# Optimization experiments

Hardware: AMD Instinct MI355X
Metric: run time of the kernel (lower is better)

The kernel has to match this reference:

```python
import jax, jax.numpy as jnp
import numpy as np

B, T, H = 4096, 512, 512
GATE = 2 + H  # concat([x(1), h(H), mask(1)])


def setup_inputs() -> dict:
    key = jax.random.key(0)
    ks = jax.random.split(key, 20)
    s = 1.0 / np.sqrt(GATE)
    inp = {
        "x": jax.random.normal(ks[0], (B, T), jnp.float32),
        "x_last": jax.random.normal(ks[1], (B, T), jnp.float32),
        "interval": jax.random.uniform(ks[2], (B, T), jnp.float32),
        "mask": (jax.random.uniform(ks[3], (B, T)) > 0.3).astype(jnp.float32),
        # gamma decay layers
        "Wgx": jax.random.normal(ks[4], (1, 1), jnp.float32),
        "bgx": jnp.zeros((1,), jnp.float32),
        "Wgh": jax.random.normal(ks[5], (H, 1), jnp.float32),
        "bgh": jnp.zeros((H,), jnp.float32),
        # gate layers: Linear(GATE, H)
        "Wz": jax.random.normal(ks[6], (H, GATE), jnp.float32) * s,
        "bz": jnp.zeros((H,), jnp.float32),
        "Wr": jax.random.normal(ks[7], (H, GATE), jnp.float32) * s,
        "br": jnp.zeros((H,), jnp.float32),
        "Wh": jax.random.normal(ks[8], (H, GATE), jnp.float32) * s,
        "bh": jnp.zeros((H,), jnp.float32),
        # output head Linear(H, 1)
        "Wo": jax.random.normal(ks[9], (1, H), jnp.float32) / np.sqrt(H),
        "bo": jnp.zeros((1,), jnp.float32),
    }
    return inp


def reference(x, x_last, interval, mask, Wgx, bgx, Wgh, bgh,
              Wz, bz, Wr, br, Wh, bh, Wo, bo):
    # x, x_last, interval, mask: [B, T]; feature dim is 1 after unsqueeze
    x3 = x[..., None]            # [B, T, 1]
    xl3 = x_last[..., None]
    it3 = interval[..., None]
    m3 = mask[..., None]
    # mean(x*m, dim=1) * T / sum(m, dim=1) == sum(x*m)/sum(m)
    x_mean = jnp.sum(x3 * m3, axis=1) / jnp.sum(m3, axis=1)  # [B, 1]

    h0 = jnp.zeros((x.shape[0], Wz.shape[0]), x.dtype)
    # time-major stacks for scan: [T, B, 1]
    xs = (jnp.swapaxes(x3, 0, 1), jnp.swapaxes(xl3, 0, 1),
          jnp.swapaxes(m3, 0, 1), jnp.swapaxes(it3, 0, 1))

    def step(h, ts):
        xt, xl, mt, it = ts  # each [B, 1]
        gamma_x = jnp.exp(-jax.nn.relu(it @ Wgx.T + bgx))   # [B, 1]
        gamma_h = jnp.exp(-jax.nn.relu(it @ Wgh.T + bgh))   # [B, H]
        xi = mt * xt + (1.0 - mt) * (gamma_x * xl + (1.0 - gamma_x) * x_mean)
        h = gamma_h * h
        comb = jnp.concatenate([xi, h, mt], axis=1)          # [B, GATE]
        z = jax.nn.sigmoid(comb @ Wz.T + bz)
        r = jax.nn.sigmoid(comb @ Wr.T + br)
        comb_r = jnp.concatenate([xi, r * h, mt], axis=1)
        h_tilde = jnp.tanh(comb_r @ Wh.T + bh)
        h = (1.0 - z) * h + z * h_tilde
        return h, None

    h, _ = jax.lax.scan(step, h0, xs)
    return jax.nn.sigmoid(h @ Wo.T + bo)  # [B, 1]
```

## Files before the change

### kernel.cpp

```cpp
#include <hip/hip_runtime.h>
#include <stdint.h>

#define T_LEN 512
#define H_DIM 512
#define B_TOT 4096
#define GATE_D 514
#define CLUSTERS 16
#define RANKS 16
#define CROWS 256
#define OWNC 32
#define NTHR 512
#define BARPAD 64

typedef short s16x8 __attribute__((ext_vector_type(8)));
typedef float f32x4 __attribute__((ext_vector_type(4)));

__device__ __forceinline__ ushort f2bf(float f) {
    uint32_t u = __builtin_bit_cast(uint32_t, f);
    u += 0x7FFF + ((u >> 16) & 1);
    return (ushort)(u >> 16);
}
__device__ __forceinline__ float sigmoid_f(float x) {
    return 1.0f / (1.0f + __expf(-x));
}
__device__ __forceinline__ float tanh_f(float x) {
    float ax = fabsf(x);
    float e  = __expf(2.0f * ax);
    float t  = 1.0f - 2.0f / (e + 1.0f);
    return copysignf(t, x);
}
__device__ __forceinline__ void vm0() {
    asm volatile("s_waitcnt vmcnt(0)" ::: "memory");
}

__global__ void k_xmean(const float* __restrict__ x, const float* __restrict__ m,
                        float* __restrict__ xmean) {
    int b = blockIdx.x;
    int l = threadIdx.x;
    const float* xr = x + (size_t)b * T_LEN;
    const float* mr = m + (size_t)b * T_LEN;
    float sx = 0.f, sm = 0.f;
    #pragma unroll
    for (int i = 0; i < T_LEN / 64; ++i) {
        float mv = mr[l + i * 64];
        sx += xr[l + i * 64] * mv;
        sm += mv;
    }
    for (int off = 32; off; off >>= 1) {
        sx += __shfl_down(sx, off);
        sm += __shfl_down(sm, off);
    }
    if (l == 0) xmean[b] = sx / sm;
}

__global__ void k_init(unsigned int* barc) {
    int i = threadIdx.x + blockIdx.x * blockDim.x;
    if (i < CLUSTERS * BARPAD) barc[i] = 0u;
}

__device__ __forceinline__ void bar_slow(unsigned int* cnt, unsigned int target) {
    vm0();
    __syncthreads();
    if (threadIdx.x == 0) {
        __builtin_amdgcn_fence(__ATOMIC_RELEASE, "agent");
        __hip_atomic_fetch_add(cnt, 1u, __ATOMIC_RELAXED, __HIP_MEMORY_SCOPE_AGENT);
        while (__hip_atomic_load(cnt, __ATOMIC_RELAXED, __HIP_MEMORY_SCOPE_AGENT) < target)
            __builtin_amdgcn_s_sleep(1);
        __builtin_amdgcn_fence(__ATOMIC_ACQUIRE, "agent");
    }
    __syncthreads();
}

__device__ __forceinline__ void bar_fast(unsigned int* cnt, unsigned int target) {
    vm0();
    __syncthreads();
    if (threadIdx.x == 0) {
        __hip_atomic_fetch_add(cnt, 1u, __ATOMIC_RELAXED, __HIP_MEMORY_SCOPE_AGENT);
        while (__hip_atomic_load(cnt, __ATOMIC_RELAXED, __HIP_MEMORY_SCOPE_AGENT) < target)
            __builtin_amdgcn_s_sleep(1);
        asm volatile("buffer_inv" ::: "memory");
        vm0();
    }
    __syncthreads();
}

__global__ __launch_bounds__(NTHR) void k_grud(
    const float* __restrict__ x,   const float* __restrict__ xl,
    const float* __restrict__ itv, const float* __restrict__ msk,
    const float* __restrict__ Wgx, const float* __restrict__ bgx,
    const float* __restrict__ Wgh, const float* __restrict__ bgh,
    const float* __restrict__ Wz,  const float* __restrict__ bz,
    const float* __restrict__ Wr,  const float* __restrict__ br,
    const float* __restrict__ Wh,  const float* __restrict__ bh,
    const float* __restrict__ Wo,  const float* __restrict__ bo,
    const float* __restrict__ xmean,
    ushort* __restrict__ hdx, ushort* __restrict__ rhx,
    float* __restrict__ osum, unsigned int* __restrict__ barc,
    float* __restrict__ out)
{
    __shared__ ushort wfrag[96 * 512];
    __shared__ ushort stage[16 * 512];
    __shared__ float  xi_s[2][CROWS], mts_s[2][CROWS], its_s[2][CROWS];
    __shared__ float4 epi_s[96];
    __shared__ float2 ghb_s[OWNC];
    __shared__ unsigned int flag_s;

    const int tid = threadIdx.x;
    const int b   = blockIdx.x;
    const int cluster = (b & 7) * 2 + ((b >> 3) >> 4);
    const int rank    = (b >> 3) & 15;
    const int wv = tid >> 6, l = tid & 63;
    const int colb = l & 15, qg = l >> 4;
    const int r0 = cluster * CROWS;

    unsigned int* cnt     = barc + cluster * BARPAD;
    unsigned int* xcd_arr = cnt + 16;
    ushort* hdc = hdx + (size_t)cluster * CROWS * H_DIM;
    ushort* rhc = rhx + (size_t)cluster * CROWS * H_DIM;
    const s16x8* WF = (const s16x8*)wfrag;
    const s16x8* HD = (const s16x8*)hdc;
    const s16x8* RH = (const s16x8*)rhc;

    for (int s = tid; s < 96 * 64; s += NTHR) {
        int fi = s >> 6, ln = s & 63;
        int g = fi >> 5, nt = (fi >> 4) & 1, kt = fi & 15;
        const float* W = (g == 0) ? Wz : (g == 1) ? Wr : Wh;
        int colg = rank * OWNC + nt * 16 + (ln & 15);
        int c0 = 1 + kt * 32 + (ln >> 4) * 8;
        ushort tb[8];
        #pragma unroll
        for (int j = 0; j < 8; ++j) tb[j] = f2bf(W[(size_t)colg * GATE_D + c0 + j]);
        *(s16x8*)&wfrag[s * 8] = *(s16x8*)tb;
    }
    for (int i = tid; i < 96; i += NTHR) {
        int g = i >> 5, c = i & 31;
        const float* W  = (g == 0) ? Wz : (g == 1) ? Wr : Wh;
        const float* bb = (g == 0) ? bz : (g == 1) ? br : bh;
        int colg = rank * OWNC + c;
        epi_s[i] = make_float4(bb[colg], W[(size_t)colg * GATE_D],
                               W[(size_t)colg * GATE_D + GATE_D - 1], 0.f);
    }
    if (tid < OWNC) ghb_s[tid] = make_float2(Wgh[rank * OWNC + tid], bgh[rank * OWNC + tid]);
    const float wgx = Wgx[0], bgx0 = bgx[0];

    #pragma unroll
    for (int i = 0; i < 2; ++i) {
        int s = tid + i * NTHR;
        *(s16x8*)((char*)hdc + ((size_t)(s >> 6) * 1024 + (size_t)rank * 64 + (s & 63)) * 16) = (s16x8){0,0,0,0,0,0,0,0};
    }

    float xmv = 0.f;
    if (tid < CROWS) {
        xmv = xmean[r0 + tid];
        size_t idx = (size_t)(r0 + tid) * T_LEN;
        float xv = x[idx], xlv = xl[idx], iv = itv[idx], mv = msk[idx];
        float gx = __expf(-fmaxf(iv * wgx + bgx0, 0.f));
        xi_s[0][tid]  = mv * xv + (1.f - mv) * (gx * xlv + (1.f - gx) * xmv);
        mts_s[0][tid] = mv;
        its_s[0][tid] = iv;
    }

    if (tid == 0) {
        unsigned int myxcc;
        asm volatile("s_getreg_b32 %0, hwreg(HW_REG_XCC_ID)" : "=s"(myxcc));
        xcd_arr[rank] = myxcc;
    }
    unsigned int ep = 1;
    bar_slow(cnt, RANKS * ep);
    if (tid == 0) {
        unsigned int x0 = xcd_arr[0], same = 1;
        #pragma unroll
        for (int rk = 1; rk < RANKS; ++rk) same &= (xcd_arr[rk] == x0) ? 1u : 0u;
        flag_s = same;
    }
    __syncthreads();
    const bool fastc = (flag_s != 0);

    float hdq[2][2][4];
    #pragma unroll
    for (int mt = 0; mt < 2; ++mt)
        #pragma unroll
        for (int nt = 0; nt < 2; ++nt)
            #pragma unroll
            for (int q = 0; q < 4; ++q) hdq[mt][nt][q] = 0.f;
    float zq[2][2][4];

    for (int t = 0; t < T_LEN; ++t) {
        const int sl = t & 1;

        f32x4 accz[2][2], accr[2][2];
        #pragma unroll
        for (int mt = 0; mt < 2; ++mt)
            #pragma unroll
            for (int nt = 0; nt < 2; ++nt) { accz[mt][nt] = (f32x4){0,0,0,0}; accr[mt][nt] = (f32x4){0,0,0,0}; }
        #pragma unroll
        for (int kt = 0; kt < 16; ++kt) {
            s16x8 a0 = HD[((2 * wv    ) * 16 + kt) * 64 + l];
            s16x8 a1 = HD[((2 * wv + 1) * 16 + kt) * 64 + l];
            #pragma unroll
            for (int nt = 0; nt < 2; ++nt) {
                s16x8 bz_ = WF[(     nt * 16 + kt) * 64 + l];
                s16x8 br_ = WF[(32 + nt * 16 + kt) * 64 + l];
                accz[0][nt] = __builtin_amdgcn_mfma_f32_16x16x32_bf16(a0, bz_, accz[0][nt], 0, 0, 0);
                accz[1][nt] = __builtin_amdgcn_mfma_f32_16x16x32_bf16(a1, bz_, accz[1][nt], 0, 0, 0);
                accr[0][nt] = __builtin_amdgcn_mfma_f32_16x16x32_bf16(a0, br_, accr[0][nt], 0, 0, 0);
                accr[1][nt] = __builtin_amdgcn_mfma_f32_16x16x32_bf16(a1, br_, accr[1][nt], 0, 0, 0);
            }
        }
        #pragma unroll
        for (int mt = 0; mt < 2; ++mt) {
            #pragma unroll
            for (int nt = 0; nt < 2; ++nt) {
                int c = nt * 16 + colb;
                float4 ez = epi_s[c];
                float4 er = epi_s[32 + c];
                int grp = (c >> 3) & 3, jj = c & 7;
                #pragma unroll
                for (int q = 0; q < 4; ++q) {
                    int row = wv * 32 + mt * 16 + qg * 4 + q;
                    float xiv = xi_s[sl][row], mtv = mts_s[sl][row];
                    zq[mt][nt][q] = sigmoid_f(accz[mt][nt][q] + ez.x + xiv * ez.y + mtv * ez.z);
                    float rr = sigmoid_f(accr[mt][nt][q] + er.x + xiv * er.y + mtv * er.z);
                    stage[(((2 * wv + mt) * 64) + (qg * 4 + q) + grp * 16) * 8 + jj] =
                        f2bf(rr * hdq[mt][nt][q]);
                }
            }
        }
        __syncthreads();
        #pragma unroll
        for (int i = 0; i < 2; ++i) {
            int s = tid + i * NTHR;
            *(s16x8*)((char*)rhc + ((size_t)(s >> 6) * 1024 + (size_t)rank * 64 + (s & 63)) * 16) =
                *(const s16x8*)&stage[s * 8];
        }
        ++ep;
        {
            unsigned int target = RANKS * ep;
            vm0();
            __syncthreads();
            if (tid == 0) {
                if (!fastc) __builtin_amdgcn_fence(__ATOMIC_RELEASE, "agent");
                __hip_atomic_fetch_add(cnt, 1u, __ATOMIC_RELAXED, __HIP_MEMORY_SCOPE_AGENT);
            }
            if (tid < CROWS && t + 1 < T_LEN) {
                size_t idx = (size_t)(r0 + tid) * T_LEN + t + 1;
                float xv = x[idx], xlv = xl[idx], iv = itv[idx], mv = msk[idx];
                float gx = __expf(-fmaxf(iv * wgx + bgx0, 0.f));
                int s2 = sl ^ 1;
                xi_s[s2][tid]  = mv * xv + (1.f - mv) * (gx * xlv + (1.f - gx) * xmv);
                mts_s[s2][tid] = mv;
                its_s[s2][tid] = iv;
            }
            if (tid == 0) {
                while (__hip_atomic_load(cnt, __ATOMIC_RELAXED, __HIP_MEMORY_SCOPE_AGENT) < target)
                    __builtin_amdgcn_s_sleep(1);
                if (fastc) { asm volatile("buffer_inv" ::: "memory"); vm0(); }
                else __builtin_amdgcn_fence(__ATOMIC_ACQUIRE, "agent");
            }
            __syncthreads();
        }

        f32x4 acc2[2][2];
        #pragma unroll
        for (int mt = 0; mt < 2; ++mt)
            #pragma unroll
            for (int nt = 0; nt < 2; ++nt) acc2[mt][nt] = (f32x4){0,0,0,0};
        #pragma unroll
        for (int kt = 0; kt < 16; ++kt) {
            s16x8 a0 = RH[((2 * wv    ) * 16 + kt) * 64 + l];
            s16x8 a1 = RH[((2 * wv + 1) * 16 + kt) * 64 + l];
            #pragma unroll
            for (int nt = 0; nt < 2; ++nt) {
                s16x8 bh_ = WF[(64 + nt * 16 + kt) * 64 + l];
                acc2[0][nt] = __builtin_amdgcn_mfma_f32_16x16x32_bf16(a0, bh_, acc2[0][nt], 0, 0, 0);
                acc2[1][nt] = __builtin_amdgcn_mfma_f32_16x16x32_bf16(a1, bh_, acc2[1][nt], 0, 0, 0);
            }
        }
        const bool last = (t + 1 == T_LEN);
        #pragma unroll
        for (int mt = 0; mt < 2; ++mt) {
            #pragma unroll
            for (int nt = 0; nt < 2; ++nt) {
                int c = nt * 16 + colb;
                float4 eh = epi_s[64 + c];
                float2 gb = ghb_s[c];
                int grp = (c >> 3) & 3, jj = c & 7;
                #pragma unroll
                for (int q = 0; q < 4; ++q) {
                    int row = wv * 32 + mt * 16 + qg * 4 + q;
                    float ht = tanh_f(acc2[mt][nt][q] + eh.x + xi_s[sl][row] * eh.y + mts_s[sl][row] * eh.z);
                    float hd = hdq[mt][nt][q];
                    float hn = hd + zq[mt][nt][q] * (ht - hd);
                    float g  = last ? 1.f : __expf(-fmaxf(its_s[sl ^ 1][row] * gb.x + gb.y, 0.f));
                    float hdn = hn * g;
                    hdq[mt][nt][q] = hdn;
                    if (!last)
                        stage[(((2 * wv + mt) * 64) + (qg * 4 + q) + grp * 16) * 8 + jj] = f2bf(hdn);
                }
            }
        }
        __syncthreads();
        if (!last) {
            #pragma unroll
            for (int i = 0; i < 2; ++i) {
                int s = tid + i * NTHR;
                *(s16x8*)((char*)hdc + ((size_t)(s >> 6) * 1024 + (size_t)rank * 64 + (s & 63)) * 16) =
                    *(const s16x8*)&stage[s * 8];
            }
        }
        ++ep;
        if (fastc) bar_fast(cnt, RANKS * ep); else bar_slow(cnt, RANKS * ep);
    }

    {
        float wo0 = Wo[rank * OWNC + colb];
        float wo1 = Wo[rank * OWNC + 16 + colb];
        #pragma unroll
        for (int mt = 0; mt < 2; ++mt) {
            #pragma unroll
            for (int q = 0; q < 4; ++q) {
                int row = wv * 32 + mt * 16 + qg * 4 + q;
                float p = hdq[mt][0][q] * wo0 + hdq[mt][1][q] * wo1;
                #pragma unroll
                for (int off = 1; off < 16; off <<= 1) p += __shfl_xor(p, off);
                if (colb == 0) osum[(size_t)(r0 + row) * RANKS + rank] = p;
            }
        }
    }
    ++ep;
    if (fastc) bar_fast(cnt, RANKS * ep); else bar_slow(cnt, RANKS * ep);
    if (rank == 0 && tid < CROWS) {
        float s = 0.f;
        #pragma unroll
        for (int rk = 0; rk < RANKS; ++rk) s += osum[(size_t)(r0 + tid) * RANKS + rk];
        out[r0 + tid] = sigmoid_f(s + bo[0]);
    }
}

extern "C" void kernel_launch(void* const* d_in, const int* in_sizes, int n_in,
                              void* d_out, int out_size, void* d_ws, size_t ws_size,
                              hipStream_t stream) {
    const float* x    = (const float*)d_in[0];
    const float* xl   = (const float*)d_in[1];
    const float* itv  = (const float*)d_in[2];
    const float* msk  = (const float*)d_in[3];
    const float* Wgx  = (const float*)d_in[4];
    const float* bgx  = (const float*)d_in[5];
    const float* Wgh  = (const float*)d_in[6];
    const float* bgh  = (const float*)d_in[7];
    const float* Wz   = (const float*)d_in[8];
    const float* bz   = (const float*)d_in[9];
    const float* Wr   = (const float*)d_in[10];
    const float* br   = (const float*)d_in[11];
    const float* Wh   = (const float*)d_in[12];
    const float* bh   = (const float*)d_in[13];
    const float* Wo   = (const float*)d_in[14];
    const float* bo   = (const float*)d_in[15];

    char* ws = (char*)d_ws;
    float*        xmean = (float*)ws;
    unsigned int* barc  = (unsigned int*)(ws + 16384);
    float*        osum  = (float*)(ws + 16384 + 4096);
    ushort*       hdx   = (ushort*)(ws + 16384 + 4096 + 262144);
    ushort*       rhx   = (ushort*)(ws + 16384 + 4096 + 262144 + 4194304);

    k_init<<<1, 1024, 0, stream>>>(barc);
    k_xmean<<<B_TOT, 64, 0, stream>>>(x, msk, xmean);
    k_grud<<<CLUSTERS * RANKS, NTHR, 0, stream>>>(
        x, xl, itv, msk, Wgx, bgx, Wgh, bgh,
        Wz, bz, Wr, br, Wh, bh, Wo, bo,
        xmean, hdx, rhx, osum, barc, (float*)d_out);
}
```

Before: 6.998 ms.

## Replace block-wide grid barriers with per-wave cross-block counters

Each wave now owns the row slice it produces and consumes, so the per-step block-level __syncthreads plus single-thread atomic barrier is replaced with per-wave arrive/wait counters shared across the 16 ranks of a cluster. Per-step inputs are loaded per wave just before the wait, which hides the load under the barrier latency and drops the double-buffered shared arrays. This removes intra-block synchronization and lets waves proceed independently. The cost is eight times more atomic traffic and spinning waves, plus a reworked barrier-memory layout.

```diff
diff --git a/kernel.cpp b/kernel.cpp
--- a/kernel.cpp
+++ b/kernel.cpp
@@ -10,7 +10,7 @@
 #define CROWS 256
 #define OWNC 32
 #define NTHR 512
-#define BARPAD 64
+#define BARPAD 256
 
 typedef short s16x8 __attribute__((ext_vector_type(8)));
 typedef float f32x4 __attribute__((ext_vector_type(4)));
@@ -71,17 +71,18 @@
     __syncthreads();
 }
 
-__device__ __forceinline__ void bar_fast(unsigned int* cnt, unsigned int target) {
+__device__ __forceinline__ void wave_arrive(unsigned int* cw, bool fastc) {
     vm0();
-    __syncthreads();
-    if (threadIdx.x == 0) {
-        __hip_atomic_fetch_add(cnt, 1u, __ATOMIC_RELAXED, __HIP_MEMORY_SCOPE_AGENT);
-        while (__hip_atomic_load(cnt, __ATOMIC_RELAXED, __HIP_MEMORY_SCOPE_AGENT) < target)
-            __builtin_amdgcn_s_sleep(1);
-        asm volatile("buffer_inv" ::: "memory");
-        vm0();
-    }
-    __syncthreads();
+    if ((threadIdx.x & 63) == 0) {
+        if (!fastc) __builtin_amdgcn_fence(__ATOMIC_RELEASE, "agent");
+        __hip_atomic_fetch_add(cw, 1u, __ATOMIC_RELAXED, __HIP_MEMORY_SCOPE_AGENT);
+    }
+}
+__device__ __forceinline__ void wave_wait(unsigned int* cw, unsigned int target, bool fastc) {
+    while (__hip_atomic_load(cw, __ATOMIC_RELAXED, __HIP_MEMORY_SCOPE_AGENT) < target)
+        __builtin_amdgcn_s_sleep(1);
+    if (fastc) { asm volatile("buffer_inv" ::: "memory"); vm0(); }
+    else __builtin_amdgcn_fence(__ATOMIC_ACQUIRE, "agent");
 }
 
 __global__ __launch_bounds__(NTHR) void k_grud(
@@ -100,7 +101,7 @@
 {
     __shared__ ushort wfrag[96 * 512];
     __shared__ ushort stage[16 * 512];
-    __shared__ float  xi_s[2][CROWS], mts_s[2][CROWS], its_s[2][CROWS];
+    __shared__ float  xi_w[8][32], mts_w[8][32], itn_w[8][32];
     __shared__ float4 epi_s[96];
     __shared__ float2 ghb_s[OWNC];
     __shared__ unsigned int flag_s;
@@ -113,8 +114,9 @@
     const int colb = l & 15, qg = l >> 4;
     const int r0 = cluster * CROWS;
 
-    unsigned int* cnt     = barc + cluster * BARPAD;
-    unsigned int* xcd_arr = cnt + 16;
+    unsigned int* base    = barc + cluster * BARPAD;
+    unsigned int* xcd_arr = base + 4;
+    unsigned int* cw      = base + 64 + wv * 16;
     ushort* hdc = hdx + (size_t)cluster * CROWS * H_DIM;
     ushort* rhc = rhx + (size_t)cluster * CROWS * H_DIM;
     const s16x8* WF = (const s16x8*)wfrag;
@@ -142,31 +144,14 @@
     }
     if (tid < OWNC) ghb_s[tid] = make_float2(Wgh[rank * OWNC + tid], bgh[rank * OWNC + tid]);
     const float wgx = Wgx[0], bgx0 = bgx[0];
-
-    #pragma unroll
-    for (int i = 0; i < 2; ++i) {
-        int s = tid + i * NTHR;
-        *(s16x8*)((char*)hdc + ((size_t)(s >> 6) * 1024 + (size_t)rank * 64 + (s & 63)) * 16) = (s16x8){0,0,0,0,0,0,0,0};
-    }
-
-    float xmv = 0.f;
-    if (tid < CROWS) {
-        xmv = xmean[r0 + tid];
-        size_t idx = (size_t)(r0 + tid) * T_LEN;
-        float xv = x[idx], xlv = xl[idx], iv = itv[idx], mv = msk[idx];
-        float gx = __expf(-fmaxf(iv * wgx + bgx0, 0.f));
-        xi_s[0][tid]  = mv * xv + (1.f - mv) * (gx * xlv + (1.f - gx) * xmv);
-        mts_s[0][tid] = mv;
-        its_s[0][tid] = iv;
-    }
+    const float xmv = (l < 32) ? xmean[r0 + wv * 32 + l] : 0.f;
 
     if (tid == 0) {
         unsigned int myxcc;
         asm volatile("s_getreg_b32 %0, hwreg(HW_REG_XCC_ID)" : "=s"(myxcc));
         xcd_arr[rank] = myxcc;
     }
-    unsigned int ep = 1;
-    bar_slow(cnt, RANKS * ep);
+    bar_slow(base, RANKS);
     if (tid == 0) {
         unsigned int x0 = xcd_arr[0], same = 1;
         #pragma unroll
@@ -175,6 +160,13 @@
     }
     __syncthreads();
     const bool fastc = (flag_s != 0);
+
+    #pragma unroll
+    for (int i = 0; i < 2; ++i) {
+        int f = 2 * wv + i;
+        *(s16x8*)((char*)hdc + (((size_t)f * 16 + rank) * 64 + l) * 16) = (s16x8){0,0,0,0,0,0,0,0};
+    }
+    wave_arrive(cw, fastc);
 
     float hdq[2][2][4];
     #pragma unroll
@@ -186,7 +178,14 @@
     float zq[2][2][4];
 
     for (int t = 0; t < T_LEN; ++t) {
-        const int sl = t & 1;
+        if (l < 32) {
+            size_t idx = (size_t)(r0 + wv * 32 + l) * T_LEN + t;
+            float xv = x[idx], xlv = xl[idx], iv = itv[idx], mv = msk[idx];
+            float gx = __expf(-fmaxf(iv * wgx + bgx0, 0.f));
+            xi_w[wv][l]  = mv * xv + (1.f - mv) * (gx * xlv + (1.f - gx) * xmv);
+            mts_w[wv][l] = mv;
+        }
+        wave_wait(cw, (unsigned int)(16 * (2 * t + 1)), fastc);
 
         f32x4 accz[2][2], accr[2][2];
         #pragma unroll
@@ -217,8 +216,8 @@
                 int grp = (c >> 3) & 3, jj = c & 7;
                 #pragma unroll
                 for (int q = 0; q < 4; ++q) {
-                    int row = wv * 32 + mt * 16 + qg * 4 + q;
-                    float xiv = xi_s[sl][row], mtv = mts_s[sl][row];
+                    int lr = mt * 16 + qg * 4 + q;
+                    float xiv = xi_w[wv][lr], mtv = mts_w[wv][lr];
                     zq[mt][nt][q] = sigmoid_f(accz[mt][nt][q] + ez.x + xiv * ez.y + mtv * ez.z);
                     float rr = sigmoid_f(accr[mt][nt][q] + er.x + xiv * er.y + mtv * er.z);
                     stage[(((2 * wv + mt) * 64) + (qg * 4 + q) + grp * 16) * 8 + jj] =
@@ -226,39 +225,17 @@
                 }
             }
         }
-        __syncthreads();
         #pragma unroll
         for (int i = 0; i < 2; ++i) {
-            int s = tid + i * NTHR;
-            *(s16x8*)((char*)rhc + ((size_t)(s >> 6) * 1024 + (size_t)rank * 64 + (s & 63)) * 16) =
-                *(const s16x8*)&stage[s * 8];
-        }
-        ++ep;
-        {
-            unsigned int target = RANKS * ep;
-            vm0();
-            __syncthreads();
-            if (tid == 0) {
-                if (!fastc) __builtin_amdgcn_fence(__ATOMIC_RELEASE, "agent");
-                __hip_atomic_fetch_add(cnt, 1u, __ATOMIC_RELAXED, __HIP_MEMORY_SCOPE_AGENT);
-            }
-            if (tid < CROWS && t + 1 < T_LEN) {
-                size_t idx = (size_t)(r0 + tid) * T_LEN + t + 1;
-                float xv = x[idx], xlv = xl[idx], iv = itv[idx], mv = msk[idx];
-                float gx = __expf(-fmaxf(iv * wgx + bgx0, 0.f));
-                int s2 = sl ^ 1;
-                xi_s[s2][tid]  = mv * xv + (1.f - mv) * (gx * xlv + (1.f - gx) * xmv);
-                mts_s[s2][tid] = mv;
-                its_s[s2][tid] = iv;
-            }
-            if (tid == 0) {
-                while (__hip_atomic_load(cnt, __ATOMIC_RELAXED, __HIP_MEMORY_SCOPE_AGENT) < target)
-                    __builtin_amdgcn_s_sleep(1);
-                if (fastc) { asm volatile("buffer_inv" ::: "memory"); vm0(); }
-                else __builtin_amdgcn_fence(__ATOMIC_ACQUIRE, "agent");
-            }
-            __syncthreads();
-        }
+            int f = 2 * wv + i;
+            *(s16x8*)((char*)rhc + (((size_t)f * 16 + rank) * 64 + l) * 16) =
+                *(const s16x8*)&stage[(f * 64 + l) * 8];
+        }
+        wave_arrive(cw, fastc);
+
+        if (l < 32 && t + 1 < T_LEN)
+            itn_w[wv][l] = itv[(size_t)(r0 + wv * 32 + l) * T_LEN + t + 1];
+        wave_wait(cw, (unsigned int)(16 * (2 * t + 2)), fastc);
 
         f32x4 acc2[2][2];
         #pragma unroll
@@ -287,11 +264,11 @@
                 int grp = (c >> 3) & 3, jj = c & 7;
                 #pragma unroll
                 for (int q = 0; q < 4; ++q) {
-                    int row = wv * 32 + mt * 16 + qg * 4 + q;
-                    float ht = tanh_f(acc2[mt][nt][q] + eh.x + xi_s[sl][row] * eh.y + mts_s[sl][row] * eh.z);
+                    int lr = mt * 16 + qg * 4 + q;
+                    float ht = tanh_f(acc2[mt][nt][q] + eh.x + xi_w[wv][lr] * eh.y + mts_w[wv][lr] * eh.z);
                     float hd = hdq[mt][nt][q];
                     float hn = hd + zq[mt][nt][q] * (ht - hd);
-                    float g  = last ? 1.f : __expf(-fmaxf(its_s[sl ^ 1][row] * gb.x + gb.y, 0.f));
+                    float g  = last ? 1.f : __expf(-fmaxf(itn_w[wv][lr] * gb.x + gb.y, 0.f));
                     float hdn = hn * g;
                     hdq[mt][nt][q] = hdn;
                     if (!last)
@@ -299,17 +276,15 @@
                 }
             }
         }
-        __syncthreads();
         if (!last) {
             #pragma unroll
             for (int i = 0; i < 2; ++i) {
-                int s = tid + i * NTHR;
-                *(s16x8*)((char*)hdc + ((size_t)(s >> 6) * 1024 + (size_t)rank * 64 + (s & 63)) * 16) =
-                    *(const s16x8*)&stage[s * 8];
-            }
-        }
-        ++ep;
-        if (fastc) bar_fast(cnt, RANKS * ep); else bar_slow(cnt, RANKS * ep);
+                int f = 2 * wv + i;
+                *(s16x8*)((char*)hdc + (((size_t)f * 16 + rank) * 64 + l) * 16) =
+                    *(const s16x8*)&stage[(f * 64 + l) * 8];
+            }
+        }
+        wave_arrive(cw, fastc);
     }
 
     {
@@ -327,8 +302,7 @@
             }
         }
     }
-    ++ep;
-    if (fastc) bar_fast(cnt, RANKS * ep); else bar_slow(cnt, RANKS * ep);
+    bar_slow(base, 2 * RANKS);
     if (rank == 0 && tid < CROWS) {
         float s = 0.f;
         #pragma unroll
@@ -360,11 +334,11 @@
     char* ws = (char*)d_ws;
     float*        xmean = (float*)ws;
     unsigned int* barc  = (unsigned int*)(ws + 16384);
-    float*        osum  = (float*)(ws + 16384 + 4096);
-    ushort*       hdx   = (ushort*)(ws + 16384 + 4096 + 262144);
-    ushort*       rhx   = (ushort*)(ws + 16384 + 4096 + 262144 + 4194304);
-
-    k_init<<<1, 1024, 0, stream>>>(barc);
+    float*        osum  = (float*)(ws + 32768);
+    ushort*       hdx   = (ushort*)(ws + 32768 + 262144);
+    ushort*       rhx   = (ushort*)(ws + 32768 + 262144 + 4194304);
+
+    k_init<<<16, 256, 0, stream>>>(barc);
     k_xmean<<<B_TOT, 64, 0, stream>>>(x, msk, xmean);
     k_grud<<<CLUSTERS * RANKS, NTHR, 0, stream>>>(
         x, xl, itv, msk, Wgx, bgx, Wgh, bgh,
```

Result: no change. 6.989 ms (-0.1%).
